# Kernel tuning notes

Hardware: AMD Instinct MI355X
Metric: run time of the kernel (lower is better)

The kernel has to match this reference:

```python
import jax, jax.numpy as jnp
import numpy as np

B_SZ, L_MAX, T_LEN, D = 512, 48, 128, 300   # sentences, graph slots, tokens, glove_dim
N_A, N_C = 2048, 2048                        # aspect rows, clause rows
H, TOP_K = 4, 96                             # attention heads, top-k over flattened LxL


def setup_inputs() -> dict:
    key = jax.random.key(0)
    ks = jax.random.split(key, 8)
    input_embed = jax.random.normal(ks[0], (B_SZ, T_LEN, D), jnp.float32)
    clause_output = jax.random.normal(ks[1], (N_C, D), jnp.float32)
    batch_aa_mask = (jax.random.uniform(ks[2], (N_A, T_LEN)) < 0.5).astype(jnp.float32)
    aa_graph_length = jax.random.randint(ks[3], (B_SZ,), 1, L_MAX + 1, dtype=jnp.int32)
    # collision-free scatter destinations; maxima hit B_SZ-1 and L_MAX-1 exactly
    map_AA = jnp.arange(N_A, dtype=jnp.int32) % B_SZ
    map_AA_idx = (4 + jnp.arange(N_A, dtype=jnp.int32) // B_SZ).at[-1].set(L_MAX - 1)
    map_AS = jnp.arange(N_C, dtype=jnp.int32) % B_SZ
    map_AS_idx = jnp.arange(N_C, dtype=jnp.int32) // B_SZ
    sc = 1.0 / np.sqrt(D).astype(np.float32)
    Wq = jax.random.normal(ks[4], (D, D), jnp.float32) * sc
    Wk = jax.random.normal(ks[5], (D, D), jnp.float32) * sc
    Wg = jax.random.normal(ks[6], (D, D), jnp.float32) * sc
    bq = jnp.zeros((D,), jnp.float32)
    bk = jnp.zeros((D,), jnp.float32)
    bg = jnp.zeros((D,), jnp.float32)
    return {"input_embed": input_embed, "clause_output": clause_output,
            "batch_aa_mask": batch_aa_mask, "aa_graph_length": aa_graph_length,
            "map_AA": map_AA, "map_AA_idx": map_AA_idx,
            "map_AS": map_AS, "map_AS_idx": map_AS_idx,
            "Wq": Wq, "bq": bq, "Wk": Wk, "bk": bk, "Wg": Wg, "bg": bg}


def reference(input_embed, clause_output, batch_aa_mask, aa_graph_length,
              map_AA, map_AA_idx, map_AS, map_AS_idx, Wq, bq, Wk, bk, Wg, bg):
    B, L = B_SZ, L_MAX
    dk = D // H
    # gather sentence tokens per aspect, masked sum over tokens -> [Na, D]
    aa_embed = jnp.einsum('ntd,nt->nd', input_embed[map_AA], batch_aa_mask)
    # scatter aspect and clause features into the [B, L, D] graph tensor
    inner = jnp.zeros((B, L, D), input_embed.dtype)
    inner = inner.at[map_AA, map_AA_idx].set(aa_embed)
    inner = inner.at[map_AS, map_AS_idx].set(clause_output)
    mask_indi = (jnp.arange(L)[None, :] < aa_graph_length[:, None]).astype(inner.dtype)  # [B,L]
    # attention-based adjacency (scores only, softmax over keys)
    q = (inner @ Wq.T + bq).reshape(B, L, H, dk).transpose(0, 2, 1, 3)
    k = (inner @ Wk.T + bk).reshape(B, L, H, dk).transpose(0, 2, 1, 3)
    scores = jnp.einsum('bhid,bhjd->bhij', q, k) / jnp.sqrt(jnp.asarray(dk, inner.dtype))
    scores = jnp.where(mask_indi[:, None, None, :] == 0, -1e9, scores)
    attn = jax.nn.softmax(scores, axis=-1)                      # [B,H,L,L]
    # average heads, replace diagonal with self-loops, zero padded rows
    adj = attn.mean(axis=1)
    eye = jnp.eye(L, dtype=adj.dtype)
    adj = adj * (1.0 - eye) + eye
    adj = adj * mask_indi[:, :, None]
    # top-k sparsify over flattened adjacency, symmetrize, diag=1, reweight
    flat = adj.reshape(B, L * L)
    kth = jax.lax.top_k(flat, TOP_K)[0][:, -1]                  # [B]
    sel = (flat >= kth[:, None]).astype(adj.dtype).reshape(B, L, L)
    sel = sel + sel.transpose(0, 2, 1)
    sel = sel * (1.0 - eye) + eye
    adj = sel * adj
    # one GCN layer: relu(W(A x) / (rowsum(A)+1))
    denom = adj.sum(axis=-1, keepdims=True) + 1.0
    gcn = jax.nn.relu((jnp.einsum('bij,bjd->bid', adj, inner) @ Wg.T + bg) / denom)
    # gather back to clause rows; keep clause_output where graph has <=1 node
    aa_out = gcn[map_AS, map_AS_idx]                            # [Nc, D]
    need = (aa_graph_length[map_AS] > 1)[:, None]
    return jnp.where(need, aa_out, clause_output)
```

## Files before the change

### kernel.cpp

```cpp
#include <hip/hip_runtime.h>
#include <math.h>

#define B_SZ 512
#define LG 48
#define T_LEN 128
#define DIM 300
#define NA 2048
#define NC 2048
#define NH 4
#define DK 75
#define KTOP 96
#define ACAP 16
#define TM 64
#define TN 64
#define KC 100
#define QKS 608
#define GTM 32
#define GTN 64
#define GKC 60
#define FCAP2 9
#define SSTR 612

__global__ __launch_bounds__(256) void build_kernel(
    const int* __restrict__ mapAA, const int* __restrict__ mapAAi,
    int* __restrict__ slot_src, int* __restrict__ acnt, int* __restrict__ alist) {
  int n = blockIdx.x * 256 + threadIdx.x;
  if (n >= NA) return;
  int b = mapAA[n];
  atomicMax(&slot_src[b * LG + mapAAi[n]], n);
  int pos = atomicAdd(&acnt[b], 1);
  if (pos < ACAP) alist[b * ACAP + pos] = n;
}

__global__ __launch_bounds__(256) void aspect_kernel(
    const float* __restrict__ embed, const float* __restrict__ mask,
    const int* __restrict__ acnt, const int* __restrict__ alist,
    float* __restrict__ X) {
  int b = blockIdx.x;
  int na = acnt[b]; if (na > ACAP) na = ACAP;
  if (na == 0) return;
  __shared__ float mLds[ACAP][T_LEN];
  __shared__ float4 eLds[32][DK];
  int tid = threadIdx.x;
  for (int i = tid; i < na * T_LEN; i += 256) {
    int k = i / T_LEN, t = i - k * T_LEN;
    mLds[k][t] = mask[(size_t)alist[b * ACAP + k] * T_LEN + t];
  }
  int nw = na * DK;
  int i0 = tid, i1 = tid + 256;
  int k0 = i0 / DK, d0 = i0 - k0 * DK;
  int k1 = i1 / DK, d1 = i1 - k1 * DK;
  float4 a0 = {0, 0, 0, 0}, a1 = {0, 0, 0, 0};
  const float4* e4 = (const float4*)(embed + (size_t)b * T_LEN * DIM);
  for (int t0 = 0; t0 < T_LEN; t0 += 32) {
    __syncthreads();
    for (int i = tid; i < 32 * DK; i += 256) {
      int t = i / DK, d = i - t * DK;
      eLds[t][d] = e4[(size_t)(t0 + t) * DK + d];
    }
    __syncthreads();
#pragma unroll
    for (int t = 0; t < 32; ++t) {
      if (i0 < nw) {
        float m = mLds[k0][t0 + t]; float4 ev = eLds[t][d0];
        a0.x += m * ev.x; a0.y += m * ev.y; a0.z += m * ev.z; a0.w += m * ev.w;
      }
      if (i1 < nw) {
        float m = mLds[k1][t0 + t]; float4 ev = eLds[t][d1];
        a1.x += m * ev.x; a1.y += m * ev.y; a1.z += m * ev.z; a1.w += m * ev.w;
      }
    }
  }
  if (i0 < nw) ((float4*)(X + (size_t)alist[b * ACAP + k0] * DIM))[d0] = a0;
  if (i1 < nw) ((float4*)(X + (size_t)alist[b * ACAP + k1] * DIM))[d1] = a1;
}

__global__ __launch_bounds__(128) void clause_kernel(
    const float* __restrict__ clause, const int* __restrict__ mapAS,
    const int* __restrict__ mapASi, float* __restrict__ X,
    int* __restrict__ slot_src) {
  int n = blockIdx.x, t = threadIdx.x;
  const float4* src = (const float4*)(clause + (size_t)n * DIM);
  float4* dst = (float4*)(X + (size_t)(NA + n) * DIM);
  if (t < DIM / 4) dst[t] = src[t];
  if (t == 96) atomicMax(&slot_src[mapAS[n] * LG + mapASi[n]], NA + n);
}

__global__ __launch_bounds__(256) void qk_kernel(
    const float* __restrict__ X, const float* __restrict__ Wq,
    const float* __restrict__ bq, const float* __restrict__ Wk,
    const float* __restrict__ bk, float* __restrict__ QK) {
  __shared__ __align__(16) float ws[TN][KC];
  int m0 = blockIdx.x * TM, n0 = blockIdx.y * TN;
  int tid = threadIdx.x;
  int ty = tid >> 4;
  int tx = tid & 15;
  float acc[4][4];
#pragma unroll
  for (int a = 0; a < 4; ++a)
#pragma unroll
    for (int c = 0; c < 4; ++c) acc[a][c] = 0.f;

  const float* xrow[4];
#pragma unroll
  for (int a = 0; a < 4; ++a) xrow[a] = X + (size_t)(m0 + ty * 4 + a) * DIM;

  for (int kc = 0; kc < DIM; kc += KC) {
    __syncthreads();
    for (int i = tid; i < TN * (KC / 4); i += 256) {
      int c = i / (KC / 4), g = i - c * (KC / 4);
      int col = n0 + c;
      float4 v = {0.f, 0.f, 0.f, 0.f};
      if (col < 2 * DIM) {
        const float* w = (col < DIM) ? (Wq + (size_t)col * DIM)
                                     : (Wk + (size_t)(col - DIM) * DIM);
        v = *(const float4*)&w[kc + g * 4];
      }
      *(float4*)&ws[c][g * 4] = v;
    }
    __syncthreads();
#pragma unroll 5
    for (int kg = 0; kg < KC / 4; ++kg) {
      float4 xv[4], wv[4];
#pragma unroll
      for (int a = 0; a < 4; ++a)
        xv[a] = *(const float4*)&xrow[a][kc + kg * 4];
#pragma unroll
      for (int c = 0; c < 4; ++c) wv[c] = *(const float4*)&ws[tx + 16 * c][kg * 4];
#pragma unroll
      for (int a = 0; a < 4; ++a)
#pragma unroll
        for (int c = 0; c < 4; ++c)
          acc[a][c] += wv[c].x * xv[a].x + wv[c].y * xv[a].y +
                       wv[c].z * xv[a].z + wv[c].w * xv[a].w;
    }
  }

#pragma unroll
  for (int cc = 0; cc < 4; ++cc) {
    int col = n0 + tx + 16 * cc;
    if (col < 2 * DIM) {
      float bias; int off;
      if (col < DIM) { bias = bq[col]; off = col + col / DK; }
      else { int c2 = col - DIM; bias = bk[c2]; off = 304 + c2 + c2 / DK; }
#pragma unroll
      for (int a = 0; a < 4; ++a)
        QK[(size_t)(m0 + ty * 4 + a) * QKS + off] = acc[a][cc] + bias;
    }
  }
}

__global__ __launch_bounds__(512) void attn2_kernel(
    const float* __restrict__ QK, const float* __restrict__ X,
    const float* __restrict__ bq, const float* __restrict__ bk,
    const int* __restrict__ slot_src, const int* __restrict__ aa_len,
    float* __restrict__ xout, float* __restrict__ dng, int* __restrict__ mdg) {
  int b = blockIdx.x, tid = threadIdx.x;
  __shared__ __align__(16) float staged[FCAP2][SSTR];
  __shared__ float buf4[NH][LG][LG + 1];
  __shared__ float coef[4][LG], denomc[4];
  __shared__ int srcs[LG], nlist[LG], flist[LG], qrow[LG];
  __shared__ float kthL;
  __shared__ int sh_nneed, sh_nf;

  int length = aa_len[b];
  if (length > LG) length = LG;
  if (tid < LG) srcs[tid] = slot_src[b * LG + tid];
  __syncthreads();

  if (tid < 64) {
    bool isneed = (tid < LG) && (srcs[tid] >= NA);
    unsigned long long nm = __ballot(isneed);
    if (isneed) nlist[__popcll(nm & ((1ull << tid) - 1ull))] = tid;
    bool isf = (tid < LG) && (srcs[tid] >= 0);
    unsigned long long fm = __ballot(isf);
    int nf = __popcll(fm);
    if (nf > FCAP2 - 1) nf = FCAP2 - 1;
    if (isf) {
      int c = __popcll(fm & ((1ull << tid) - 1ull));
      if (c < FCAP2 - 1) flist[c] = tid;
    }
    if (tid < LG) {
      int c = __popcll(fm & ((1ull << tid) - 1ull));
      qrow[tid] = (isf && c < FCAP2 - 1) ? c : nf;
    }
    if (tid == 0) { sh_nneed = __popcll(nm); sh_nf = nf; }
  }
  __syncthreads();
  int nneed = sh_nneed, nf = sh_nf;

  if (length <= 1) {
    if (tid < nneed) mdg[srcs[nlist[tid]] - NA] = 0;
    return;
  }

  for (int i = tid; i < nf * 152; i += 512) {
    int m = i / 152, g = i - m * 152;
    ((float4*)staged[m])[g] =
        ((const float4*)(QK + (size_t)srcs[flist[m]] * QKS))[g];
  }
  for (int j = tid; j < 608; j += 512) {
    int half = (j >= 304) ? 1 : 0;
    int jj = j - half * 304;
    int h = jj / 76, d = jj - h * 76;
    float v = 0.f;
    if (d < DK) v = half ? bk[h * DK + d] : bq[h * DK + d];
    staged[nf][j] = v;
  }
  __syncthreads();
  if (tid < nf * 8) {
    int m = tid >> 3, p = tid & 7;
    int pos = (p & 3) * 76 + 75 + ((p >> 2) * 304);
    staged[m][pos] = 0.f;
  }
  __syncthreads();

  const float sdk = sqrtf((float)DK);
  int h = tid >> 7;
  int t = tid & 127;
  int ti = t >> 3, tj = t & 7;
  int i0 = ti * 3, j0 = tj * 6;

  int qr[3], kr[6];
#pragma unroll
  for (int a = 0; a < 3; ++a) qr[a] = qrow[i0 + a];
#pragma unroll
  for (int c = 0; c < 6; ++c) kr[c] = qrow[j0 + c];

  if (i0 < length) {
    float acc[3][6];
#pragma unroll
    for (int a = 0; a < 3; ++a)
#pragma unroll
      for (int c = 0; c < 6; ++c) acc[a][c] = 0.f;
    for (int d4 = 0; d4 < 19; ++d4) {
      float4 qv[3], kv[6];
#pragma unroll
      for (int a = 0; a < 3; ++a)
        qv[a] = *(const float4*)&staged[qr[a]][h * 76 + d4 * 4];
#pragma unroll
      for (int c = 0; c < 6; ++c)
        kv[c] = *(const float4*)&staged[kr[c]][304 + h * 76 + d4 * 4];
#pragma unroll
      for (int a = 0; a < 3; ++a)
#pragma unroll
        for (int c = 0; c < 6; ++c)
          acc[a][c] += qv[a].x * kv[c].x + qv[a].y * kv[c].y +
                       qv[a].z * kv[c].z + qv[a].w * kv[c].w;
    }
#pragma unroll
    for (int a = 0; a < 3; ++a) {
      float p[6];
#pragma unroll
      for (int c = 0; c < 6; ++c)
        p[c] = (j0 + c < length) ? (acc[a][c] / sdk) : -1e9f;
      float mx = p[0];
#pragma unroll
      for (int c = 1; c < 6; ++c) mx = fmaxf(mx, p[c]);
      mx = fmaxf(mx, __shfl_xor(mx, 1));
      mx = fmaxf(mx, __shfl_xor(mx, 2));
      mx = fmaxf(mx, __shfl_xor(mx, 4));
      float rs = 0.f;
#pragma unroll
      for (int c = 0; c < 6; ++c) { p[c] = expf(p[c] - mx); rs += p[c]; }
      rs += __shfl_xor(rs, 1);
      rs += __shfl_xor(rs, 2);
      rs += __shfl_xor(rs, 4);
      if (i0 + a < length) {
#pragma unroll
        for (int c = 0; c < 6; ++c)
          buf4[h][i0 + a][j0 + c] = p[c] / rs;
      }
    }
  }
  __syncthreads();

  for (int e = tid; e < LG * LG; e += 512) {
    int i = e / LG, j = e - (e / LG) * LG;
    float v = 0.f;
    if (i < length)
      v = ((buf4[0][i][j] + buf4[1][i][j]) +
           (buf4[2][i][j] + buf4[3][i][j])) * 0.25f;
    if (i == j) v = (i < length) ? 1.0f : 0.0f;
    buf4[0][i][j] = v;
  }
  __syncthreads();

  if (tid < 64) {
    unsigned int vb[36];
#pragma unroll
    for (int v = 0; v < 36; ++v) {
      int e = v * 64 + tid;
      vb[v] = __float_as_uint(buf4[0][e / LG][e % LG]);
    }
    unsigned int cur = 0u;
    for (int bit = 30; bit >= 0; --bit) {
      unsigned int cand = cur | (1u << bit);
      int c = 0;
#pragma unroll
      for (int v = 0; v < 36; ++v) c += (vb[v] >= cand) ? 1 : 0;
      c += __shfl_xor(c, 32); c += __shfl_xor(c, 16);
      c += __shfl_xor(c, 8);  c += __shfl_xor(c, 4);
      c += __shfl_xor(c, 2);  c += __shfl_xor(c, 1);
      if (c >= KTOP) cur = cand;
    }
    if (tid == 0) kthL = __uint_as_float(cur);
  }
  __syncthreads();
  const float kth = kthL;

  int nc = (nneed > 4) ? 4 : nneed;
  if (tid < nc * LG) {
    int r = tid / LG, j = tid - (tid / LG) * LG;
    int i = nlist[r];
    float aij = buf4[0][i][j];
    float v;
    if (j == i) v = aij;
    else {
      float selv = (aij >= kth ? 1.f : 0.f) + (buf4[0][j][i] >= kth ? 1.f : 0.f);
      v = selv * aij;
    }
    coef[r][j] = v;
  }
  __syncthreads();
  if (tid < nc) {
    float sm = 0.f;
    for (int j = 0; j < LG; ++j) sm += coef[tid][j];
    denomc[tid] = sm + 1.f;
  }
  __syncthreads();
  for (int w = tid; w < nc * (DIM / 4); w += 512) {
    int r = w / (DIM / 4), d4 = w - (w / (DIM / 4)) * (DIM / 4);
    float4 acc = {0.f, 0.f, 0.f, 0.f};
    for (int m = 0; m < nf; ++m) {
      int j = flist[m];
      float a = coef[r][j];
      float4 xv = ((const float4*)(X + (size_t)srcs[j] * DIM))[d4];
      acc.x += a * xv.x; acc.y += a * xv.y;
      acc.z += a * xv.z; acc.w += a * xv.w;
    }
    int n = srcs[nlist[r]] - NA;
    ((float4*)(xout + (size_t)n * DIM))[d4] = acc;
  }
  if (tid < nc) {
    int n = srcs[nlist[tid]] - NA;
    mdg[n] = 1;
    dng[n] = denomc[tid];
  }
}

__global__ __launch_bounds__(256) void gcn_kernel(
    const float* __restrict__ xg, const float* __restrict__ dng,
    const int* __restrict__ mdg, const float* __restrict__ Wg,
    const float* __restrict__ bg, const float* __restrict__ clause,
    float* __restrict__ out) {
  __shared__ __align__(16) float xs[GTM][GKC];
  __shared__ __align__(16) float ws[GTN][GKC];
  int m0 = blockIdx.x * GTM, n0 = blockIdx.y * GTN;
  int tid = threadIdx.x;
  int ty = tid >> 4;
  int tx = tid & 15;
  float acc[2][4];
#pragma unroll
  for (int a = 0; a < 2; ++a)
#pragma unroll
    for (int c = 0; c < 4; ++c) acc[a][c] = 0.f;

  for (int kc = 0; kc < DIM; kc += GKC) {
    __syncthreads();
    for (int i = tid; i < GTM * (GKC / 4); i += 256) {
      int r = i / (GKC / 4), g = i - r * (GKC / 4);
      *(float4*)&xs[r][g * 4] =
          *(const float4*)&xg[(size_t)(m0 + r) * DIM + kc + g * 4];
    }
    for (int i = tid; i < GTN * (GKC / 4); i += 256) {
      int c = i / (GKC / 4), g = i - c * (GKC / 4);
      int col = n0 + c;
      float4 v = {0.f, 0.f, 0.f, 0.f};
      if (col < DIM)
        v = *(const float4*)&Wg[(size_t)col * DIM + kc + g * 4];
      *(float4*)&ws[c][g * 4] = v;
    }
    __syncthreads();
#pragma unroll 5
    for (int kg = 0; kg < GKC / 4; ++kg) {
      float4 xv[2], wv[4];
#pragma unroll
      for (int a = 0; a < 2; ++a) xv[a] = *(const float4*)&xs[ty * 2 + a][kg * 4];
#pragma unroll
      for (int c = 0; c < 4; ++c) wv[c] = *(const float4*)&ws[tx + 16 * c][kg * 4];
#pragma unroll
      for (int a = 0; a < 2; ++a)
#pragma unroll
        for (int c = 0; c < 4; ++c)
          acc[a][c] += wv[c].x * xv[a].x + wv[c].y * xv[a].y +
                       wv[c].z * xv[a].z + wv[c].w * xv[a].w;
    }
  }

  int md[2]; float dn[2];
#pragma unroll
  for (int a = 0; a < 2; ++a) {
    int row = m0 + ty * 2 + a;
    md[a] = mdg[row];
    dn[a] = dng[row];
  }
#pragma unroll
  for (int cc = 0; cc < 4; ++cc) {
    int col = n0 + tx + 16 * cc;
    if (col < DIM) {
      float bgc = bg[col];
#pragma unroll
      for (int a = 0; a < 2; ++a) {
        int row = m0 + ty * 2 + a;
        float v;
        if (md[a]) v = fmaxf((acc[a][cc] + bgc) / dn[a], 0.f);
        else v = clause[(size_t)row * DIM + col];
        out[(size_t)row * DIM + col] = v;
      }
    }
  }
}

extern "C" void kernel_launch(void* const* d_in, const int* in_sizes, int n_in,
                              void* d_out, int out_size, void* d_ws, size_t ws_size,
                              hipStream_t stream) {
  (void)in_sizes; (void)n_in; (void)out_size; (void)ws_size;
  const float* input_embed = (const float*)d_in[0];
  const float* clause      = (const float*)d_in[1];
  const float* aa_mask     = (const float*)d_in[2];
  const int*   aa_len      = (const int*)d_in[3];
  const int*   map_AA      = (const int*)d_in[4];
  const int*   map_AA_idx  = (const int*)d_in[5];
  const int*   map_AS      = (const int*)d_in[6];
  const int*   map_AS_idx  = (const int*)d_in[7];
  const float* Wq = (const float*)d_in[8];
  const float* bq = (const float*)d_in[9];
  const float* Wk = (const float*)d_in[10];
  const float* bk = (const float*)d_in[11];
  const float* Wg = (const float*)d_in[12];
  const float* bg = (const float*)d_in[13];
  float* out = (float*)d_out;

  float* X  = (float*)d_ws;
  float* QK = X + (size_t)(NA + NC) * DIM;
  int* slot_src = (int*)(QK + (size_t)(NA + NC) * QKS);
  int* acnt = slot_src + B_SZ * LG;
  int* alist = acnt + B_SZ;
  float* dng = (float*)alist;
  int* mdg = (int*)(dng + NC);
  float* xg = (float*)(alist + B_SZ * ACAP);

  hipMemsetAsync(slot_src, 0xFF, (size_t)B_SZ * LG * sizeof(int), stream);
  hipMemsetAsync(acnt, 0x00, (size_t)B_SZ * sizeof(int), stream);
  build_kernel<<<(NA + 255) / 256, 256, 0, stream>>>(map_AA, map_AA_idx,
                                                     slot_src, acnt, alist);
  clause_kernel<<<NC, 128, 0, stream>>>(clause, map_AS, map_AS_idx, X, slot_src);
  aspect_kernel<<<B_SZ, 256, 0, stream>>>(input_embed, aa_mask, acnt, alist, X);
  dim3 qkgrid((NA + NC) / TM, (2 * DIM + TN - 1) / TN);
  qk_kernel<<<qkgrid, 256, 0, stream>>>(X, Wq, bq, Wk, bk, QK);
  attn2_kernel<<<B_SZ, 512, 0, stream>>>(QK, X, bq, bk, slot_src, aa_len,
                                         xg, dng, mdg);
  dim3 ggrid(NC / GTM, (DIM + GTN - 1) / GTN);
  gcn_kernel<<<ggrid, 256, 0, stream>>>(xg, dng, mdg, Wg, bg, clause, out);
}
```

Baseline: 152.8 us.

## Split QK projection K-dimension across two grid slices, reduce partials in attention

The QK projection GEMM now splits the 300-wide reduction into two halves along blockIdx.z. Each block loads its whole half of the weight tile into shared memory once, which removes the chunked loop and its per-chunk syncs. Each half writes a separate partial buffer, and the attention kernel sums the two partials and adds the bias while staging rows. This doubles the grid for better occupancy, but it doubles the QK write traffic and adds a second read in the attention kernel.

```diff
diff --git a/kernel.cpp b/kernel.cpp
--- a/kernel.cpp
+++ b/kernel.cpp
@@ -13,7 +13,7 @@
 #define ACAP 16
 #define TM 64
 #define TN 64
-#define KC 100
+#define WSS 156
 #define QKS 608
 #define GTM 32
 #define GTN 64
@@ -88,9 +88,11 @@
 
 __global__ __launch_bounds__(256) void qk_kernel(
     const float* __restrict__ X, const float* __restrict__ Wq,
-    const float* __restrict__ bq, const float* __restrict__ Wk,
-    const float* __restrict__ bk, float* __restrict__ QK) {
-  __shared__ __align__(16) float ws[TN][KC];
+    const float* __restrict__ Wk, float* __restrict__ QKP) {
+  __shared__ __align__(16) float ws[TN][WSS];
+  int z = blockIdx.z;
+  int kbase = z ? 152 : 0;
+  int ng = z ? 37 : 38;
   int m0 = blockIdx.x * TM, n0 = blockIdx.y * TN;
   int tid = threadIdx.x;
   int ty = tid >> 4;
@@ -101,57 +103,56 @@
 #pragma unroll
     for (int c = 0; c < 4; ++c) acc[a][c] = 0.f;
 
+  for (int i = tid; i < TN * ng; i += 256) {
+    int c = i / ng, g = i - c * ng;
+    int col = n0 + c;
+    float4 v = {0.f, 0.f, 0.f, 0.f};
+    if (col < 2 * DIM) {
+      const float* w = (col < DIM) ? (Wq + (size_t)col * DIM)
+                                   : (Wk + (size_t)(col - DIM) * DIM);
+      v = *(const float4*)&w[kbase + g * 4];
+    }
+    *(float4*)&ws[c][g * 4] = v;
+  }
+  __syncthreads();
+
   const float* xrow[4];
 #pragma unroll
-  for (int a = 0; a < 4; ++a) xrow[a] = X + (size_t)(m0 + ty * 4 + a) * DIM;
-
-  for (int kc = 0; kc < DIM; kc += KC) {
-    __syncthreads();
-    for (int i = tid; i < TN * (KC / 4); i += 256) {
-      int c = i / (KC / 4), g = i - c * (KC / 4);
-      int col = n0 + c;
-      float4 v = {0.f, 0.f, 0.f, 0.f};
-      if (col < 2 * DIM) {
-        const float* w = (col < DIM) ? (Wq + (size_t)col * DIM)
-                                     : (Wk + (size_t)(col - DIM) * DIM);
-        v = *(const float4*)&w[kc + g * 4];
-      }
-      *(float4*)&ws[c][g * 4] = v;
-    }
-    __syncthreads();
-#pragma unroll 5
-    for (int kg = 0; kg < KC / 4; ++kg) {
-      float4 xv[4], wv[4];
-#pragma unroll
-      for (int a = 0; a < 4; ++a)
-        xv[a] = *(const float4*)&xrow[a][kc + kg * 4];
-#pragma unroll
-      for (int c = 0; c < 4; ++c) wv[c] = *(const float4*)&ws[tx + 16 * c][kg * 4];
-#pragma unroll
-      for (int a = 0; a < 4; ++a)
-#pragma unroll
-        for (int c = 0; c < 4; ++c)
-          acc[a][c] += wv[c].x * xv[a].x + wv[c].y * xv[a].y +
-                       wv[c].z * xv[a].z + wv[c].w * xv[a].w;
-    }
-  }
-
+  for (int a = 0; a < 4; ++a)
+    xrow[a] = X + (size_t)(m0 + ty * 4 + a) * DIM + kbase;
+
+#pragma unroll 2
+  for (int kg = 0; kg < ng; ++kg) {
+    float4 xv[4], wv[4];
+#pragma unroll
+    for (int a = 0; a < 4; ++a) xv[a] = *(const float4*)&xrow[a][kg * 4];
+#pragma unroll
+    for (int c = 0; c < 4; ++c) wv[c] = *(const float4*)&ws[tx + 16 * c][kg * 4];
+#pragma unroll
+    for (int a = 0; a < 4; ++a)
+#pragma unroll
+      for (int c = 0; c < 4; ++c)
+        acc[a][c] += wv[c].x * xv[a].x + wv[c].y * xv[a].y +
+                     wv[c].z * xv[a].z + wv[c].w * xv[a].w;
+  }
+
+  float* out = QKP + (size_t)z * (NA + NC) * QKS;
 #pragma unroll
   for (int cc = 0; cc < 4; ++cc) {
     int col = n0 + tx + 16 * cc;
     if (col < 2 * DIM) {
-      float bias; int off;
-      if (col < DIM) { bias = bq[col]; off = col + col / DK; }
-      else { int c2 = col - DIM; bias = bk[c2]; off = 304 + c2 + c2 / DK; }
+      int off;
+      if (col < DIM) off = col + col / DK;
+      else { int c2 = col - DIM; off = 304 + c2 + c2 / DK; }
 #pragma unroll
       for (int a = 0; a < 4; ++a)
-        QK[(size_t)(m0 + ty * 4 + a) * QKS + off] = acc[a][cc] + bias;
+        out[(size_t)(m0 + ty * 4 + a) * QKS + off] = acc[a][cc];
     }
   }
 }
 
 __global__ __launch_bounds__(512) void attn2_kernel(
-    const float* __restrict__ QK, const float* __restrict__ X,
+    const float* __restrict__ QKP, const float* __restrict__ X,
     const float* __restrict__ bq, const float* __restrict__ bk,
     const int* __restrict__ slot_src, const int* __restrict__ aa_len,
     float* __restrict__ xout, float* __restrict__ dng, int* __restrict__ mdg) {
@@ -194,11 +195,6 @@
     return;
   }
 
-  for (int i = tid; i < nf * 152; i += 512) {
-    int m = i / 152, g = i - m * 152;
-    ((float4*)staged[m])[g] =
-        ((const float4*)(QK + (size_t)srcs[flist[m]] * QKS))[g];
-  }
   for (int j = tid; j < 608; j += 512) {
     int half = (j >= 304) ? 1 : 0;
     int jj = j - half * 304;
@@ -206,6 +202,24 @@
     float v = 0.f;
     if (d < DK) v = half ? bk[h * DK + d] : bq[h * DK + d];
     staged[nf][j] = v;
+  }
+  __syncthreads();
+  {
+    const float* P0 = QKP;
+    const float* P1 = QKP + (size_t)(NA + NC) * QKS;
+    for (int i = tid; i < nf * 152; i += 512) {
+      int m = i / 152, g = i - m * 152;
+      size_t base = (size_t)srcs[flist[m]] * QKS + g * 4;
+      float4 a = *(const float4*)&P0[base];
+      float4 c = *(const float4*)&P1[base];
+      float4 bv = *(const float4*)&staged[nf][g * 4];
+      float4 v;
+      v.x = (a.x + c.x) + bv.x;
+      v.y = (a.y + c.y) + bv.y;
+      v.z = (a.z + c.z) + bv.z;
+      v.w = (a.w + c.w) + bv.w;
+      *(float4*)&staged[m][g * 4] = v;
+    }
   }
   __syncthreads();
   if (tid < nf * 8) {
@@ -442,9 +456,9 @@
   const float* bg = (const float*)d_in[13];
   float* out = (float*)d_out;
 
-  float* X  = (float*)d_ws;
-  float* QK = X + (size_t)(NA + NC) * DIM;
-  int* slot_src = (int*)(QK + (size_t)(NA + NC) * QKS);
+  float* X   = (float*)d_ws;
+  float* QKP = X + (size_t)(NA + NC) * DIM;
+  int* slot_src = (int*)(QKP + (size_t)2 * (NA + NC) * QKS);
   int* acnt = slot_src + B_SZ * LG;
   int* alist = acnt + B_SZ;
   float* dng = (float*)alist;
@@ -457,9 +471,9 @@
                                                      slot_src, acnt, alist);
   clause_kernel<<<NC, 128, 0, stream>>>(clause, map_AS, map_AS_idx, X, slot_src);
   aspect_kernel<<<B_SZ, 256, 0, stream>>>(input_embed, aa_mask, acnt, alist, X);
-  dim3 qkgrid((NA + NC) / TM, (2 * DIM + TN - 1) / TN);
-  qk_kernel<<<qkgrid, 256, 0, stream>>>(X, Wq, bq, Wk, bk, QK);
-  attn2_kernel<<<B_SZ, 512, 0, stream>>>(QK, X, bq, bk, slot_src, aa_len,
+  dim3 qkgrid((NA + NC) / TM, (2 * DIM + TN - 1) / TN, 2);
+  qk_kernel<<<qkgrid, 256, 0, stream>>>(X, Wq, Wk, QKP);
+  attn2_kernel<<<B_SZ, 512, 0, stream>>>(QKP, X, bq, bk, slot_src, aa_len,
                                          xg, dng, mdg);
   dim3 ggrid(NC / GTM, (DIM + GTN - 1) / GTN);
   gcn_kernel<<<ggrid, 256, 0, stream>>>(xg, dng, mdg, Wg, bg, clause, out);
```

After: 148.6 us (median of 2 runs). -2.8%, faster.
